# Kernel tuning notes

Measured on AMD Instinct MI355X. Metric: run time of the kernel, lower is better.

## Reference

```python
import jax, jax.numpy as jnp
import numpy as np

B = 16384
D1 = 256
D2 = 256
D_FF = 1024
N_BINS = 16
TAIL = 3.0
MIN_VAL = 1e-3
MIN_TOTAL = N_BINS * MIN_VAL
TAIL_CONST = float(np.log(np.exp(1.0 - MIN_VAL) - 1.0))
D_OUT = (3 * N_BINS - 1) * D2  # 12032


def setup_inputs() -> dict:
    key = jax.random.key(0)
    ks = jax.random.split(key, 8)
    s = lambda fan: 1.0 / np.sqrt(fan)
    return {
        'x1': jax.random.normal(ks[0], (B, D1), jnp.float32),
        'x2': jax.random.normal(ks[1], (B, D2), jnp.float32),
        'W0': jax.random.normal(ks[2], (D1, D_FF), jnp.float32) * s(D1),
        'b0': jnp.zeros((D_FF,), jnp.float32),
        'W1': jax.random.normal(ks[3], (D_FF, D_FF), jnp.float32) * s(D_FF),
        'b1': jnp.zeros((D_FF,), jnp.float32),
        'W2': jax.random.normal(ks[4], (D_FF, D_OUT), jnp.float32) * s(D_FF),
        'b2': jnp.zeros((D_OUT,), jnp.float32),
    }


def _rqs_forward(x, wu, hu, du):
    # x: [B, D2]; wu, hu: [B, D2, N_BINS]; du: [B, D2, N_BINS-1]
    widths = MIN_VAL + (1.0 - MIN_TOTAL) * jax.nn.softmax(wu, axis=-1)
    heights = MIN_VAL + (1.0 - MIN_TOTAL) * jax.nn.softmax(hu, axis=-1)
    cw = jnp.cumsum(widths, axis=-1)
    cw = jnp.concatenate([jnp.zeros_like(cw[..., :1]), cw], axis=-1)
    cw = 2.0 * TAIL * cw - TAIL  # x bin edges in [-TAIL, TAIL], [B,D2,N_BINS+1]
    ch = jnp.cumsum(heights, axis=-1)
    ch = jnp.concatenate([jnp.zeros_like(ch[..., :1]), ch], axis=-1)
    ch = 2.0 * TAIL * ch - TAIL  # y bin edges
    w = cw[..., 1:] - cw[..., :-1]
    h = ch[..., 1:] - ch[..., :-1]
    # boundary derivatives padded so softplus(TAIL_CONST)+MIN_VAL == 1 (linear tails)
    pad = jnp.full_like(du[..., :1], TAIL_CONST)
    d = MIN_VAL + jax.nn.softplus(jnp.concatenate([pad, du, pad], axis=-1))  # [B,D2,N_BINS+1]
    inside = (x > -TAIL) & (x < TAIL)
    xc = jnp.clip(x, -TAIL, TAIL)
    # data-dependent bin search against interior edges
    idx = jnp.sum((xc[..., None] >= cw[..., 1:-1]).astype(jnp.int32), axis=-1)  # [B,D2]
    take = lambda a: jnp.take_along_axis(a, idx[..., None], axis=-1)[..., 0]
    xk = take(cw[..., :-1]); yk = take(ch[..., :-1])
    wk = take(w); hk = take(h)
    dk = take(d[..., :-1]); dk1 = take(d[..., 1:])
    sk = hk / wk
    theta = (xc - xk) / wk
    t1m = theta * (1.0 - theta)
    denom = sk + (dk + dk1 - 2.0 * sk) * t1m
    y = yk + hk * (sk * theta * theta + dk * t1m) / denom
    deriv = sk * sk * (dk1 * theta * theta + 2.0 * sk * t1m + dk * (1.0 - theta) ** 2) / (denom * denom)
    y = jnp.where(inside, y, x)            # identity tails
    logdet = jnp.where(inside, jnp.log(deriv), 0.0)
    return y, jnp.sum(logdet, axis=-1)     # [B,D2], [B]


def reference(x1, x2, W0, b0, W1, b1, W2, b2):
    # conditioner MLP: x1 -> spline parameters
    hdn = jax.nn.relu(x1 @ W0 + b0)
    hdn = jax.nn.relu(hdn @ W1 + b1)
    p = (hdn @ W2 + b2).reshape(-1, D2, 3 * N_BINS - 1)
    wu = p[..., :N_BINS]
    hu = p[..., N_BINS:2 * N_BINS]
    du = p[..., 2 * N_BINS:]
    y2, logdet = _rqs_forward(x2, wu, hu, du)
    return y2, logdet
```

## Files before the change

kernel.cpp:

```cpp
#include <hip/hip_runtime.h>
#include <math.h>

using u16 = unsigned short;
using bf16x8 = __attribute__((ext_vector_type(8))) short;
using f32x4  = __attribute__((ext_vector_type(4))) float;

#define DEV static __device__ __forceinline__

DEV u16 f2bf(float f) {
  union { float f; unsigned u; } v; v.f = f;
  unsigned u = v.u + 0x7fffu + ((v.u >> 16) & 1u);
  return (u16)(u >> 16);
}

DEV void gload16(const void* g, void* l) {
  __builtin_amdgcn_global_load_lds(
      (const __attribute__((address_space(1))) void*)g,
      (__attribute__((address_space(3))) void*)l, 16, 0, 0);
}

__global__ void k_conv_bf16(const float* __restrict__ in, u16* __restrict__ out, int n) {
  int i = blockIdx.x * 256 + threadIdx.x;
  if (i < n) out[i] = f2bf(in[i]);
}

__global__ void k_transconv(const float* __restrict__ in, u16* __restrict__ out,
                            int K, int Nin, int Nout, int pack) {
  __shared__ float t[32][33];
  int kb = blockIdx.x * 32, nb = blockIdx.y * 32;
  int tx = threadIdx.x & 31, ty = threadIdx.x >> 5;
  #pragma unroll
  for (int i = 0; i < 4; ++i) {
    int k = kb + ty + i * 8;
    int no = nb + tx;
    float v = 0.f;
    if (k < K && no < Nout) {
      if (pack) {
        int r = no % 48;
        if (r < 47) v = in[(size_t)k * Nin + (no / 48) * 47 + r];
      } else {
        v = in[(size_t)k * Nin + no];
      }
    }
    t[ty + i * 8][tx] = v;
  }
  __syncthreads();
  #pragma unroll
  for (int i = 0; i < 4; ++i) {
    int no = nb + ty + i * 8;
    int k = kb + tx;
    if (no < Nout && k < K) out[(size_t)no * K + k] = f2bf(t[tx][ty + i * 8]);
  }
}

__global__ __launch_bounds__(256)
void k_gemm_relu(const u16* __restrict__ A, const u16* __restrict__ Bt,
                 const float* __restrict__ bias, u16* __restrict__ C,
                 int N, int K) {
  constexpr int BM = 128, BN = 128, BK = 32;
  __shared__ __align__(16) u16 lds[(BM + BN) * BK];
  int tid = threadIdx.x, w = tid >> 6, lane = tid & 63;
  int bn = blockIdx.x, bm = blockIdx.y;
  int brow = bm * BM, bcol = bn * BN;
  int wm = w >> 1, wn = w & 1;
  int fr = lane & 15, fg = lane >> 4;
  f32x4 acc[4][4];
  #pragma unroll
  for (int i = 0; i < 4; ++i)
    #pragma unroll
    for (int j = 0; j < 4; ++j) acc[i][j] = (f32x4){0.f, 0.f, 0.f, 0.f};

  constexpr int ACH = BM * BK / 8;
  constexpr int CALLS = (BM + BN) * BK / 8 / 64;

  for (int kt = 0; kt < K; kt += BK) {
    for (int j = 0; j * 4 + w < CALLS; ++j) {
      int cb = (j * 4 + w) * 64;
      int c = cb + lane;
      const u16* g;
      if (c < ACH) {
        int row = c >> 2, c8 = c & 3;
        g = A + (size_t)(brow + row) * K + kt + c8 * 8;
      } else {
        int b = c - ACH;
        int nn = b >> 2, c8 = b & 3;
        g = Bt + (size_t)(bcol + nn) * K + kt + c8 * 8;
      }
      gload16(g, &lds[cb * 8]);
    }
    asm volatile("s_waitcnt vmcnt(0)" ::: "memory");
    __syncthreads();

    const u16* Al = lds;
    const u16* Bl = lds + BM * BK;
    bf16x8 af[4], bfr[4];
    #pragma unroll
    for (int mi = 0; mi < 4; ++mi)
      af[mi] = *(const bf16x8*)&Al[(wm * 64 + mi * 16 + fr) * BK + fg * 8];
    #pragma unroll
    for (int ni = 0; ni < 4; ++ni)
      bfr[ni] = *(const bf16x8*)&Bl[(wn * 64 + ni * 16 + fr) * BK + fg * 8];
    #pragma unroll
    for (int mi = 0; mi < 4; ++mi)
      #pragma unroll
      for (int ni = 0; ni < 4; ++ni)
        acc[mi][ni] = __builtin_amdgcn_mfma_f32_16x16x32_bf16(af[mi], bfr[ni], acc[mi][ni], 0, 0, 0);
    __syncthreads();
  }

  #pragma unroll
  for (int ni = 0; ni < 4; ++ni) {
    int col = bcol + wn * 64 + ni * 16 + fr;
    float bb = bias[col];
    #pragma unroll
    for (int mi = 0; mi < 4; ++mi) {
      #pragma unroll
      for (int q = 0; q < 4; ++q) {
        int row = brow + wm * 64 + mi * 16 + fg * 4 + q;
        float vv = acc[mi][ni][q] + bb;
        C[(size_t)row * N + col] = f2bf(vv > 0.f ? vv : 0.f);
      }
    }
  }
}

__global__ __launch_bounds__(512, 4)
void k_gemm3_fused(const u16* __restrict__ A, const u16* __restrict__ Bt,
                   const float* __restrict__ b2, const float* __restrict__ x2,
                   float* __restrict__ y2, float* __restrict__ ldpart) {
  extern __shared__ char smem[];
  const int tid = threadIdx.x, w = tid >> 6, lane = tid & 63;
  const int wm = w >> 2, wn = w & 3;
  const int fr = lane & 15, fg = lane >> 4;

  const int bid = blockIdx.x;
  const int bm = bid >> 6;
  const int bn = ((bid & 7) << 3) | ((bid >> 3) & 7);
  const int brow = bm * 256;

  const int csrc = (tid & 3) ^ ((tid >> 2) & 3);
  const u16* gA0 = A + (size_t)(brow + (tid >> 2)) * 1024 + csrc * 8;
  const u16* gB0 = Bt + (size_t)(bn * 192 + (tid >> 2)) * 1024 + csrc * 8;

#define ISSUE_ALL(t1) {                                              \
    const size_t ko_ = (size_t)(t1) * 32;                            \
    char* pa_ = smem + ((t1) & 1) * 16384;                           \
    char* pb_ = smem + 32768 + ((t1) & 1) * 12288;                   \
    gload16(gA0 + ko_, pa_ + tid * 16);                              \
    gload16(gA0 + 131072 + ko_, pa_ + tid * 16 + 8192);              \
    if (w < 6) {                                                     \
      gload16(gB0 + ko_, pb_ + tid * 16);                            \
      gload16(gB0 + 98304 + ko_, pb_ + tid * 16 + 6144);             \
    } }

  const int sc = ((fg ^ (fr & 3)) << 4);

  f32x4 acc[8][3];
  #pragma unroll
  for (int m = 0; m < 8; ++m)
    #pragma unroll
    for (int n = 0; n < 3; ++n) acc[m][n] = (f32x4){0.f, 0.f, 0.f, 0.f};

  ISSUE_ALL(0);
  asm volatile("s_waitcnt vmcnt(0)" ::: "memory");
  __syncthreads();

  for (int t = 0; t < 32; ++t) {
    if (t < 31) ISSUE_ALL(t + 1);
    const char* Ab = smem + (t & 1) * 16384;
    const char* Bb = smem + 32768 + (t & 1) * 12288;
    bf16x8 b[3];
    #pragma unroll
    for (int n = 0; n < 3; ++n)
      b[n] = *(const bf16x8*)(Bb + (wn * 48 + n * 16 + fr) * 64 + sc);
    __builtin_amdgcn_s_setprio(1);
    #pragma unroll
    for (int m = 0; m < 8; ++m) {
      bf16x8 a = *(const bf16x8*)(Ab + (wm * 128 + m * 16 + fr) * 64 + sc);
      #pragma unroll
      for (int n = 0; n < 3; ++n)
        acc[m][n] = __builtin_amdgcn_mfma_f32_16x16x32_bf16(a, b[n], acc[m][n], 0, 0, 0);
    }
    __builtin_amdgcn_s_setprio(0);
    asm volatile("s_waitcnt vmcnt(0)" ::: "memory");
    __syncthreads();
  }

  float* ldacc = (float*)(smem + 50176);
  #pragma unroll
  for (int round = 0; round < 4; ++round) {
    const int W = round >> 1, rh = round & 1;
    if (wm == W) {
      float* slot = (float*)(smem + wn * 12544);
      #pragma unroll
      for (int mm = 0; mm < 4; ++mm)
        #pragma unroll
        for (int n = 0; n < 3; ++n)
          #pragma unroll
          for (int q = 0; q < 4; ++q)
            slot[(mm * 16 + fg * 4 + q) * 49 + n * 16 + fr] = acc[rh * 4 + mm][n][q];
    }
    __syncthreads();
    if (tid < 256) {
      const int grp = tid >> 6, r = tid & 63;
      const float* pr = (const float*)(smem + grp * 12544) + r * 49;
      const int grow = brow + W * 128 + rh * 64 + r;
      const int d2 = bn * 4 + grp;
      const float* bb = b2 + (size_t)d2 * 47;

      float wv[16], hv[16];
      #pragma unroll
      for (int j = 0; j < 16; ++j) wv[j] = pr[j] + bb[j];
      #pragma unroll
      for (int j = 0; j < 16; ++j) hv[j] = pr[16 + j] + bb[16 + j];

      float x = x2[(size_t)grow * 256 + d2];
      float xc = fminf(fmaxf(x, -3.f), 3.f);

      float mw = wv[0];
      #pragma unroll
      for (int j = 1; j < 16; ++j) mw = fmaxf(mw, wv[j]);
      float sw = 0.f;
      #pragma unroll
      for (int j = 0; j < 16; ++j) { wv[j] = __expf(wv[j] - mw); sw += wv[j]; }
      float scw = 0.984f / sw;

      float mh = hv[0];
      #pragma unroll
      for (int j = 1; j < 16; ++j) mh = fmaxf(mh, hv[j]);
      float sh = 0.f;
      #pragma unroll
      for (int j = 0; j < 16; ++j) { hv[j] = __expf(hv[j] - mh); sh += hv[j]; }
      float sch = 0.984f / sh;

      int idx = 0;
      float xk = -3.f, cum = 0.f;
      #pragma unroll
      for (int i = 1; i <= 15; ++i) {
        cum += 0.001f + wv[i - 1] * scw;
        float cwi = 6.f * cum - 3.f;
        if (xc >= cwi) { idx = i; xk = cwi; }
      }
      float yk = -3.f, cumh = 0.f;
      #pragma unroll
      for (int i = 1; i <= 15; ++i) {
        cumh += 0.001f + hv[i - 1] * sch;
        float chi = 6.f * cumh - 3.f;
        if (i == idx) yk = chi;
      }
      float wk = 1.f, hk = 1.f;
      #pragma unroll
      for (int i = 0; i < 16; ++i) {
        if (i == idx) {
          wk = 6.f * (0.001f + wv[i] * scw);
          hk = 6.f * (0.001f + hv[i] * sch);
        }
      }
      float dk = 1.f, dk1 = 1.f;
      #pragma unroll
      for (int i = 1; i <= 15; ++i) {
        float u = pr[32 + i - 1] + bb[32 + i - 1];
        float e = __expf(u);
        float dd = 0.001f + (u > 15.f ? u : log1pf(e));
        if (i == idx) dk = dd;
        if (i == idx + 1) dk1 = dd;
      }

      float sk = hk / wk;
      float th = (xc - xk) / wk;
      float om = 1.f - th;
      float t1m = th * om;
      float den = sk + (dk + dk1 - 2.f * sk) * t1m;
      float y = yk + hk * (sk * th * th + dk * t1m) / den;
      float deriv = sk * sk * (dk1 * th * th + 2.f * sk * t1m + dk * om * om) / (den * den);
      bool inside = (x > -3.f) && (x < 3.f);
      float yout = inside ? y : x;
      float ld = inside ? __logf(deriv) : 0.f;

      y2[(size_t)grow * 256 + d2] = yout;
      ldacc[(W * 128 + rh * 64 + r) * 4 + grp] = ld;
    }
    __syncthreads();
  }

  if (tid < 256) {
    float s = ldacc[tid * 4] + ldacc[tid * 4 + 1] + ldacc[tid * 4 + 2] + ldacc[tid * 4 + 3];
    ldpart[(size_t)bn * 16384 + brow + tid] = s;
  }
}

__global__ void k_reduce_ld(const float* __restrict__ part, float* __restrict__ out) {
  int r = blockIdx.x * 256 + threadIdx.x;
  float s = 0.f;
  for (int j = 0; j < 64; ++j) s += part[(size_t)j * 16384 + r];
  out[r] = s;
}

extern "C" void kernel_launch(void* const* d_in, const int* in_sizes, int n_in,
                              void* d_out, int out_size, void* d_ws, size_t ws_size,
                              hipStream_t stream) {
  const float* x1 = (const float*)d_in[0];
  const float* x2 = (const float*)d_in[1];
  const float* W0 = (const float*)d_in[2];
  const float* b0 = (const float*)d_in[3];
  const float* W1 = (const float*)d_in[4];
  const float* b1 = (const float*)d_in[5];
  const float* W2 = (const float*)d_in[6];
  const float* b2 = (const float*)d_in[7];
  float* y2 = (float*)d_out;
  float* logdet = y2 + (size_t)16384 * 256;

  char* ws = (char*)d_ws;
  u16* W2t = (u16*)ws;
  u16* W0t = (u16*)(ws + 25165824);
  u16* W1t = (u16*)(ws + 25165824 + 524288);
  u16* x1b = (u16*)(ws + 27787264);
  float* ldp = (float*)(ws + 27787264);
  u16* h1  = (u16*)(ws + 36175872);
  u16* h2  = (u16*)(ws + 69730304);

  hipFuncSetAttribute((const void*)k_gemm3_fused,
                      hipFuncAttributeMaxDynamicSharedMemorySize, 57344);

  k_conv_bf16<<<16384, 256, 0, stream>>>(x1, x1b, 16384 * 256);
  k_transconv<<<dim3(8, 32), 256, 0, stream>>>(W0, W0t, 256, 1024, 1024, 0);
  k_transconv<<<dim3(32, 32), 256, 0, stream>>>(W1, W1t, 1024, 1024, 1024, 0);
  k_transconv<<<dim3(32, 384), 256, 0, stream>>>(W2, W2t, 1024, 12032, 12288, 1);

  k_gemm_relu<<<dim3(8, 128), 256, 0, stream>>>(x1b, W0t, b0, h1, 1024, 256);
  k_gemm_relu<<<dim3(8, 128), 256, 0, stream>>>(h1, W1t, b1, h2, 1024, 1024);
  k_gemm3_fused<<<4096, 512, 57344, stream>>>(h2, W2t, b2, x2, y2, ldp);
  k_reduce_ld<<<64, 256, 0, stream>>>(ldp, logdet);
}
```

Before: 866.4 us.

## Retile final fused GEMM to 128x192 blocks with 256 threads and BK=64

The last GEMM with the fused spline epilogue now uses 128-row by 192-column tiles with 4 waves instead of 256x192 with 8 waves. The K step doubles to 64, with an 8-way XOR swizzle, which halves the loop iterations and barriers. Each wave now computes a 64x96 sub-tile, raising MFMA work per LDS read, and all 256 threads take part in the spline epilogue. In exchange, LDS per block grows to 80KB, which limits occupancy, and each B tile is read from global memory twice as often.

```diff
diff --git a/kernel.cpp b/kernel.cpp
--- a/kernel.cpp
+++ b/kernel.cpp
@@ -124,62 +124,79 @@
   }
 }
 
-__global__ __launch_bounds__(512, 4)
+__global__ __launch_bounds__(256, 2)
 void k_gemm3_fused(const u16* __restrict__ A, const u16* __restrict__ Bt,
                    const float* __restrict__ b2, const float* __restrict__ x2,
                    float* __restrict__ y2, float* __restrict__ ldpart) {
   extern __shared__ char smem[];
   const int tid = threadIdx.x, w = tid >> 6, lane = tid & 63;
-  const int wm = w >> 2, wn = w & 3;
+  const int wm = w >> 1, wn = w & 1;
   const int fr = lane & 15, fg = lane >> 4;
 
   const int bid = blockIdx.x;
   const int bm = bid >> 6;
   const int bn = ((bid & 7) << 3) | ((bid >> 3) & 7);
-  const int brow = bm * 256;
-
-  const int csrc = (tid & 3) ^ ((tid >> 2) & 3);
-  const u16* gA0 = A + (size_t)(brow + (tid >> 2)) * 1024 + csrc * 8;
-  const u16* gB0 = Bt + (size_t)(bn * 192 + (tid >> 2)) * 1024 + csrc * 8;
-
-#define ISSUE_ALL(t1) {                                              \
-    const size_t ko_ = (size_t)(t1) * 32;                            \
-    char* pa_ = smem + ((t1) & 1) * 16384;                           \
-    char* pb_ = smem + 32768 + ((t1) & 1) * 12288;                   \
-    gload16(gA0 + ko_, pa_ + tid * 16);                              \
-    gload16(gA0 + 131072 + ko_, pa_ + tid * 16 + 8192);              \
-    if (w < 6) {                                                     \
-      gload16(gB0 + ko_, pb_ + tid * 16);                            \
-      gload16(gB0 + 98304 + ko_, pb_ + tid * 16 + 6144);             \
-    } }
-
-  const int sc = ((fg ^ (fr & 3)) << 4);
-
-  f32x4 acc[8][3];
-  #pragma unroll
-  for (int m = 0; m < 8; ++m)
-    #pragma unroll
-    for (int n = 0; n < 3; ++n) acc[m][n] = (f32x4){0.f, 0.f, 0.f, 0.f};
+  const int brow = bm * 128;
+
+  const int csrc = (tid & 7) ^ ((tid >> 3) & 7);
+  const u16* gA[4]; const u16* gB[6];
+  #pragma unroll
+  for (int k = 0; k < 4; ++k)
+    gA[k] = A + (size_t)(brow + (tid >> 3) + 32 * k) * 1024 + csrc * 8;
+  #pragma unroll
+  for (int k = 0; k < 6; ++k)
+    gB[k] = Bt + (size_t)(bn * 192 + (tid >> 3) + 32 * k) * 1024 + csrc * 8;
+
+#define ISSUE_ALL(t1) {                                               \
+    const size_t ko_ = (size_t)(t1) * 64;                             \
+    char* pa_ = smem + ((t1) & 1) * 16384;                            \
+    char* pb_ = smem + 32768 + ((t1) & 1) * 24576;                    \
+    gload16(gA[0] + ko_, pa_ + tid * 16);                             \
+    gload16(gA[1] + ko_, pa_ + tid * 16 + 4096);                      \
+    gload16(gA[2] + ko_, pa_ + tid * 16 + 8192);                      \
+    gload16(gA[3] + ko_, pa_ + tid * 16 + 12288);                     \
+    gload16(gB[0] + ko_, pb_ + tid * 16);                             \
+    gload16(gB[1] + ko_, pb_ + tid * 16 + 4096);                      \
+    gload16(gB[2] + ko_, pb_ + tid * 16 + 8192);                      \
+    gload16(gB[3] + ko_, pb_ + tid * 16 + 12288);                     \
+    gload16(gB[4] + ko_, pb_ + tid * 16 + 16384);                     \
+    gload16(gB[5] + ko_, pb_ + tid * 16 + 20480); }
+
+  const int sc0 = ((fg ^ (fr & 7)) << 4);
+  const int sc1 = (((4 + fg) ^ (fr & 7)) << 4);
+
+  f32x4 acc[4][6];
+  #pragma unroll
+  for (int m = 0; m < 4; ++m)
+    #pragma unroll
+    for (int n = 0; n < 6; ++n) acc[m][n] = (f32x4){0.f, 0.f, 0.f, 0.f};
 
   ISSUE_ALL(0);
   asm volatile("s_waitcnt vmcnt(0)" ::: "memory");
   __syncthreads();
 
-  for (int t = 0; t < 32; ++t) {
-    if (t < 31) ISSUE_ALL(t + 1);
+  for (int t = 0; t < 16; ++t) {
+    if (t < 15) ISSUE_ALL(t + 1);
     const char* Ab = smem + (t & 1) * 16384;
-    const char* Bb = smem + 32768 + (t & 1) * 12288;
-    bf16x8 b[3];
-    #pragma unroll
-    for (int n = 0; n < 3; ++n)
-      b[n] = *(const bf16x8*)(Bb + (wn * 48 + n * 16 + fr) * 64 + sc);
+    const char* Bb = smem + 32768 + (t & 1) * 24576;
+    bf16x8 b0[6], b1[6];
+    #pragma unroll
+    for (int n = 0; n < 6; ++n) {
+      const char* bp = Bb + (wn * 96 + n * 16 + fr) * 128;
+      b0[n] = *(const bf16x8*)(bp + sc0);
+      b1[n] = *(const bf16x8*)(bp + sc1);
+    }
     __builtin_amdgcn_s_setprio(1);
     #pragma unroll
-    for (int m = 0; m < 8; ++m) {
-      bf16x8 a = *(const bf16x8*)(Ab + (wm * 128 + m * 16 + fr) * 64 + sc);
-      #pragma unroll
-      for (int n = 0; n < 3; ++n)
-        acc[m][n] = __builtin_amdgcn_mfma_f32_16x16x32_bf16(a, b[n], acc[m][n], 0, 0, 0);
+    for (int m = 0; m < 4; ++m) {
+      const char* ap = Ab + (wm * 64 + m * 16 + fr) * 128;
+      bf16x8 a0 = *(const bf16x8*)(ap + sc0);
+      bf16x8 a1 = *(const bf16x8*)(ap + sc1);
+      #pragma unroll
+      for (int n = 0; n < 6; ++n) {
+        acc[m][n] = __builtin_amdgcn_mfma_f32_16x16x32_bf16(a0, b0[n], acc[m][n], 0, 0, 0);
+        acc[m][n] = __builtin_amdgcn_mfma_f32_16x16x32_bf16(a1, b1[n], acc[m][n], 0, 0, 0);
+      }
     }
     __builtin_amdgcn_s_setprio(0);
     asm volatile("s_waitcnt vmcnt(0)" ::: "memory");
@@ -187,25 +204,27 @@
   }
 
   float* ldacc = (float*)(smem + 50176);
-  #pragma unroll
-  for (int round = 0; round < 4; ++round) {
-    const int W = round >> 1, rh = round & 1;
-    if (wm == W) {
-      float* slot = (float*)(smem + wn * 12544);
-      #pragma unroll
-      for (int mm = 0; mm < 4; ++mm)
+  float* fl = (float*)smem;
+  #pragma unroll
+  for (int rh = 0; rh < 2; ++rh) {
+    if (wm == rh) {
+      #pragma unroll
+      for (int m = 0; m < 4; ++m)
         #pragma unroll
-        for (int n = 0; n < 3; ++n)
+        for (int n = 0; n < 6; ++n) {
+          const int g = wn * 2 + (n >= 3 ? 1 : 0);
+          const int ci = (n % 3) * 16 + fr;
           #pragma unroll
           for (int q = 0; q < 4; ++q)
-            slot[(mm * 16 + fg * 4 + q) * 49 + n * 16 + fr] = acc[rh * 4 + mm][n][q];
-    }
-    __syncthreads();
-    if (tid < 256) {
-      const int grp = tid >> 6, r = tid & 63;
-      const float* pr = (const float*)(smem + grp * 12544) + r * 49;
-      const int grow = brow + W * 128 + rh * 64 + r;
-      const int d2 = bn * 4 + grp;
+            fl[g * 3136 + (m * 16 + fg * 4 + q) * 49 + ci] = acc[m][n][q];
+        }
+    }
+    __syncthreads();
+    {
+      const int g = tid >> 6, r = tid & 63;
+      const float* pr = fl + g * 3136 + r * 49;
+      const int grow = brow + rh * 64 + r;
+      const int d2 = bn * 4 + g;
       const float* bb = b2 + (size_t)d2 * 47;
 
       float wv[16], hv[16];
@@ -278,12 +297,12 @@
       float ld = inside ? __logf(deriv) : 0.f;
 
       y2[(size_t)grow * 256 + d2] = yout;
-      ldacc[(W * 128 + rh * 64 + r) * 4 + grp] = ld;
-    }
-    __syncthreads();
-  }
-
-  if (tid < 256) {
+      ldacc[(rh * 64 + r) * 4 + g] = ld;
+    }
+    __syncthreads();
+  }
+
+  if (tid < 128) {
     float s = ldacc[tid * 4] + ldacc[tid * 4 + 1] + ldacc[tid * 4 + 2] + ldacc[tid * 4 + 3];
     ldpart[(size_t)bn * 16384 + brow + tid] = s;
   }
@@ -320,7 +339,7 @@
   u16* h2  = (u16*)(ws + 69730304);
 
   hipFuncSetAttribute((const void*)k_gemm3_fused,
-                      hipFuncAttributeMaxDynamicSharedMemorySize, 57344);
+                      hipFuncAttributeMaxDynamicSharedMemorySize, 81920);
 
   k_conv_bf16<<<16384, 256, 0, stream>>>(x1, x1b, 16384 * 256);
   k_transconv<<<dim3(8, 32), 256, 0, stream>>>(W0, W0t, 256, 1024, 1024, 0);
@@ -329,6 +348,6 @@
 
   k_gemm_relu<<<dim3(8, 128), 256, 0, stream>>>(x1b, W0t, b0, h1, 1024, 256);
   k_gemm_relu<<<dim3(8, 128), 256, 0, stream>>>(h1, W1t, b1, h2, 1024, 1024);
-  k_gemm3_fused<<<4096, 512, 57344, stream>>>(h2, W2t, b2, x2, y2, ldp);
+  k_gemm3_fused<<<8192, 256, 81920, stream>>>(h2, W2t, b2, x2, y2, ldp);
   k_reduce_ld<<<64, 256, 0, stream>>>(ldp, logdet);
 }
```

New measurement: 736.4 us. 1.18x faster.

## Restructure final GEMM into a 192x192 tile with a three-stage 64-wide K pipeline

Applied to the files above, without the earlier changes.

Changes the fused third GEMM from 256x192 tiles with a double-buffered 32-wide K loop to 192x192 tiles with a triple-buffered 64-wide K pipeline. The wait before each barrier now only drains to vmcnt(6), so one stage's loads stay in flight during the next compute. The tile is square, the grid grows to 5504 blocks with clamping and guards on the ragged last row block, and the epilogue now handles 384 rows per round in two rounds. The kernel needs 144KB of LDS, which allows only one block per CU, so it gives up occupancy in exchange for deeper prefetch and fewer barriers.

```diff
diff --git a/kernel.cpp b/kernel.cpp
--- a/kernel.cpp
+++ b/kernel.cpp
@@ -124,7 +124,7 @@
   }
 }
 
-__global__ __launch_bounds__(512, 4)
+__global__ __launch_bounds__(512, 1)
 void k_gemm3_fused(const u16* __restrict__ A, const u16* __restrict__ Bt,
                    const float* __restrict__ b2, const float* __restrict__ x2,
                    float* __restrict__ y2, float* __restrict__ ldpart) {
@@ -136,76 +136,101 @@
   const int bid = blockIdx.x;
   const int bm = bid >> 6;
   const int bn = ((bid & 7) << 3) | ((bid >> 3) & 7);
-  const int brow = bm * 256;
-
-  const int csrc = (tid & 3) ^ ((tid >> 2) & 3);
-  const u16* gA0 = A + (size_t)(brow + (tid >> 2)) * 1024 + csrc * 8;
-  const u16* gB0 = Bt + (size_t)(bn * 192 + (tid >> 2)) * 1024 + csrc * 8;
-
-#define ISSUE_ALL(t1) {                                              \
-    const size_t ko_ = (size_t)(t1) * 32;                            \
-    char* pa_ = smem + ((t1) & 1) * 16384;                           \
-    char* pb_ = smem + 32768 + ((t1) & 1) * 12288;                   \
-    gload16(gA0 + ko_, pa_ + tid * 16);                              \
-    gload16(gA0 + 131072 + ko_, pa_ + tid * 16 + 8192);              \
-    if (w < 6) {                                                     \
-      gload16(gB0 + ko_, pb_ + tid * 16);                            \
-      gload16(gB0 + 98304 + ko_, pb_ + tid * 16 + 6144);             \
-    } }
-
-  const int sc = ((fg ^ (fr & 3)) << 4);
-
-  f32x4 acc[8][3];
-  #pragma unroll
-  for (int m = 0; m < 8; ++m)
+  const int brow = bm * 192;
+
+  const int csrc = (tid & 7) ^ ((tid >> 3) & 7);
+  const u16* gA[3]; const u16* gB[3];
+  #pragma unroll
+  for (int u = 0; u < 3; ++u) {
+    int rowA = brow + (tid >> 3) + 64 * u;
+    rowA = rowA < 16383 ? rowA : 16383;
+    gA[u] = A + (size_t)rowA * 1024 + csrc * 8;
+    gB[u] = Bt + (size_t)(bn * 192 + (tid >> 3) + 64 * u) * 1024 + csrc * 8;
+  }
+  const int ldst = tid * 16;
+
+#define STAGE(t1, sbase) {                                           \
+    const size_t ko_ = (size_t)(t1) * 64;                            \
+    char* p_ = smem + (sbase);                                       \
+    gload16(gA[0] + ko_, p_ + ldst);                                 \
+    gload16(gA[1] + ko_, p_ + 8192 + ldst);                          \
+    gload16(gA[2] + ko_, p_ + 16384 + ldst);                         \
+    gload16(gB[0] + ko_, p_ + 24576 + ldst);                         \
+    gload16(gB[1] + ko_, p_ + 32768 + ldst);                         \
+    gload16(gB[2] + ko_, p_ + 40960 + ldst); }
+
+  const int sc0 = ((fg ^ (fr & 7)) << 4);
+  const int sc1 = (((4 + fg) ^ (fr & 7)) << 4);
+
+  f32x4 acc[6][3];
+  #pragma unroll
+  for (int m = 0; m < 6; ++m)
     #pragma unroll
     for (int n = 0; n < 3; ++n) acc[m][n] = (f32x4){0.f, 0.f, 0.f, 0.f};
 
-  ISSUE_ALL(0);
-  asm volatile("s_waitcnt vmcnt(0)" ::: "memory");
+#define COMPUTE(sbase) {                                             \
+    const char* Ab_ = smem + (sbase);                                \
+    const char* Bb_ = smem + (sbase) + 24576;                        \
+    bf16x8 b0[3], b1[3];                                             \
+    _Pragma("unroll")                                                \
+    for (int n_ = 0; n_ < 3; ++n_) {                                 \
+      const char* bp_ = Bb_ + (wn * 48 + n_ * 16 + fr) * 128;        \
+      b0[n_] = *(const bf16x8*)(bp_ + sc0);                          \
+      b1[n_] = *(const bf16x8*)(bp_ + sc1);                          \
+    }                                                                \
+    __builtin_amdgcn_s_setprio(1);                                   \
+    _Pragma("unroll")                                                \
+    for (int m_ = 0; m_ < 6; ++m_) {                                 \
+      const char* ap_ = Ab_ + (wm * 96 + m_ * 16 + fr) * 128;        \
+      bf16x8 a0_ = *(const bf16x8*)(ap_ + sc0);                      \
+      bf16x8 a1_ = *(const bf16x8*)(ap_ + sc1);                      \
+      _Pragma("unroll")                                              \
+      for (int n_ = 0; n_ < 3; ++n_) {                               \
+        acc[m_][n_] = __builtin_amdgcn_mfma_f32_16x16x32_bf16(a0_, b0[n_], acc[m_][n_], 0, 0, 0); \
+        acc[m_][n_] = __builtin_amdgcn_mfma_f32_16x16x32_bf16(a1_, b1[n_], acc[m_][n_], 0, 0, 0); \
+      }                                                              \
+    }                                                                \
+    __builtin_amdgcn_s_setprio(0); }
+
+#define VMW(n) asm volatile("s_waitcnt vmcnt(" #n ")" ::: "memory")
+
+  STAGE(0, 0); STAGE(1, 49152);
+  VMW(6);
+  __builtin_amdgcn_s_barrier();
+
+  for (int j = 0; j < 4; ++j) {
+    const int t = j * 3;
+    STAGE(t + 2, 98304); COMPUTE(0);     VMW(6); __builtin_amdgcn_s_barrier();
+    STAGE(t + 3, 0);     COMPUTE(49152); VMW(6); __builtin_amdgcn_s_barrier();
+    STAGE(t + 4, 49152); COMPUTE(98304); VMW(6); __builtin_amdgcn_s_barrier();
+  }
+  STAGE(14, 98304); COMPUTE(0); VMW(6); __builtin_amdgcn_s_barrier();
+  STAGE(15, 0);     COMPUTE(49152); VMW(6); __builtin_amdgcn_s_barrier();
+  COMPUTE(98304); VMW(0); __builtin_amdgcn_s_barrier();
+  COMPUTE(0);
   __syncthreads();
 
-  for (int t = 0; t < 32; ++t) {
-    if (t < 31) ISSUE_ALL(t + 1);
-    const char* Ab = smem + (t & 1) * 16384;
-    const char* Bb = smem + 32768 + (t & 1) * 12288;
-    bf16x8 b[3];
-    #pragma unroll
-    for (int n = 0; n < 3; ++n)
-      b[n] = *(const bf16x8*)(Bb + (wn * 48 + n * 16 + fr) * 64 + sc);
-    __builtin_amdgcn_s_setprio(1);
-    #pragma unroll
-    for (int m = 0; m < 8; ++m) {
-      bf16x8 a = *(const bf16x8*)(Ab + (wm * 128 + m * 16 + fr) * 64 + sc);
-      #pragma unroll
-      for (int n = 0; n < 3; ++n)
-        acc[m][n] = __builtin_amdgcn_mfma_f32_16x16x32_bf16(a, b[n], acc[m][n], 0, 0, 0);
-    }
-    __builtin_amdgcn_s_setprio(0);
-    asm volatile("s_waitcnt vmcnt(0)" ::: "memory");
-    __syncthreads();
-  }
-
-  float* ldacc = (float*)(smem + 50176);
-  #pragma unroll
-  for (int round = 0; round < 4; ++round) {
-    const int W = round >> 1, rh = round & 1;
-    if (wm == W) {
-      float* slot = (float*)(smem + wn * 12544);
-      #pragma unroll
-      for (int mm = 0; mm < 4; ++mm)
+  float* fl = (float*)smem;
+  float* ldacc = (float*)(smem + 75264);
+  #pragma unroll
+  for (int r = 0; r < 2; ++r) {
+    if ((wn >> 1) == r) {
+      float* slot = fl + (wn & 1) * 9408;
+      #pragma unroll
+      for (int m = 0; m < 6; ++m)
         #pragma unroll
         for (int n = 0; n < 3; ++n)
           #pragma unroll
           for (int q = 0; q < 4; ++q)
-            slot[(mm * 16 + fg * 4 + q) * 49 + n * 16 + fr] = acc[rh * 4 + mm][n][q];
+            slot[(wm * 96 + m * 16 + fg * 4 + q) * 49 + n * 16 + fr] = acc[m][n][q];
     }
     __syncthreads();
-    if (tid < 256) {
-      const int grp = tid >> 6, r = tid & 63;
-      const float* pr = (const float*)(smem + grp * 12544) + r * 49;
-      const int grow = brow + W * 128 + rh * 64 + r;
-      const int d2 = bn * 4 + grp;
+    if (tid < 384) {
+      const int g01 = (tid >= 192) ? 1 : 0;
+      const int rr = tid - g01 * 192;
+      const int grow = brow + rr;
+      const int d2 = bn * 4 + r * 2 + g01;
+      const float* pr = fl + g01 * 9408 + rr * 49;
       const float* bb = b2 + (size_t)d2 * 47;
 
       float wv[16], hv[16];
@@ -214,7 +239,7 @@
       #pragma unroll
       for (int j = 0; j < 16; ++j) hv[j] = pr[16 + j] + bb[16 + j];
 
-      float x = x2[(size_t)grow * 256 + d2];
+      float x = (grow < 16384) ? x2[(size_t)grow * 256 + d2] : 0.f;
       float xc = fminf(fmaxf(x, -3.f), 3.f);
 
       float mw = wv[0];
@@ -277,15 +302,20 @@
       float yout = inside ? y : x;
       float ld = inside ? __logf(deriv) : 0.f;
 
-      y2[(size_t)grow * 256 + d2] = yout;
-      ldacc[(W * 128 + rh * 64 + r) * 4 + grp] = ld;
+      if (grow < 16384) {
+        y2[(size_t)grow * 256 + d2] = yout;
+        ldacc[rr * 4 + r * 2 + g01] = ld;
+      }
     }
     __syncthreads();
   }
 
-  if (tid < 256) {
-    float s = ldacc[tid * 4] + ldacc[tid * 4 + 1] + ldacc[tid * 4 + 2] + ldacc[tid * 4 + 3];
-    ldpart[(size_t)bn * 16384 + brow + tid] = s;
+  if (tid < 192) {
+    int grow = brow + tid;
+    if (grow < 16384) {
+      float s = ldacc[tid * 4] + ldacc[tid * 4 + 1] + ldacc[tid * 4 + 2] + ldacc[tid * 4 + 3];
+      ldpart[(size_t)bn * 16384 + grow] = s;
+    }
   }
 }
 
@@ -320,7 +350,7 @@
   u16* h2  = (u16*)(ws + 69730304);
 
   hipFuncSetAttribute((const void*)k_gemm3_fused,
-                      hipFuncAttributeMaxDynamicSharedMemorySize, 57344);
+                      hipFuncAttributeMaxDynamicSharedMemorySize, 147456);
 
   k_conv_bf16<<<16384, 256, 0, stream>>>(x1, x1b, 16384 * 256);
   k_transconv<<<dim3(8, 32), 256, 0, stream>>>(W0, W0t, 256, 1024, 1024, 0);
@@ -329,6 +359,6 @@
 
   k_gemm_relu<<<dim3(8, 128), 256, 0, stream>>>(x1b, W0t, b0, h1, 1024, 256);
   k_gemm_relu<<<dim3(8, 128), 256, 0, stream>>>(h1, W1t, b1, h2, 1024, 1024);
-  k_gemm3_fused<<<4096, 512, 57344, stream>>>(h2, W2t, b2, x2, y2, ldp);
+  k_gemm3_fused<<<5504, 512, 147456, stream>>>(h2, W2t, b2, x2, y2, ldp);
   k_reduce_ld<<<64, 256, 0, stream>>>(ldp, logdet);
 }
```

After: 889.3 us. 2.6% more time.

## Enlarge fused GEMM3 tile to 256x384 with 1024 threads and triple-buffered LDS

Applied to the files above, without the earlier changes.

The fused output GEMM now uses 1024-thread blocks computing 256x384 tiles (eight spline dims per block instead of four), halving the number of blocks and the partial log-det columns. Global-to-LDS loads move from double to triple buffering with partial vmcnt waits, so the next two stages stay in flight during compute, and the LDS swizzle changes to suit the new layout. The spline epilogue is split across 512 threads in four rounds. This raises arithmetic intensity and load/compute overlap, at the cost of 120KB LDS per block, which leaves one block per CU and fewer blocks overall.

```diff
diff --git a/kernel.cpp b/kernel.cpp
--- a/kernel.cpp
+++ b/kernel.cpp
@@ -124,7 +124,7 @@
   }
 }
 
-__global__ __launch_bounds__(512, 4)
+__global__ __launch_bounds__(1024, 4)
 void k_gemm3_fused(const u16* __restrict__ A, const u16* __restrict__ Bt,
                    const float* __restrict__ b2, const float* __restrict__ x2,
                    float* __restrict__ y2, float* __restrict__ ldpart) {
@@ -134,78 +134,90 @@
   const int fr = lane & 15, fg = lane >> 4;
 
   const int bid = blockIdx.x;
-  const int bm = bid >> 6;
-  const int bn = ((bid & 7) << 3) | ((bid >> 3) & 7);
+  const int bm = bid >> 5;
+  const int bn = ((bid & 7) << 2) | ((bid >> 3) & 3);
   const int brow = bm * 256;
 
-  const int csrc = (tid & 3) ^ ((tid >> 2) & 3);
-  const u16* gA0 = A + (size_t)(brow + (tid >> 2)) * 1024 + csrc * 8;
-  const u16* gB0 = Bt + (size_t)(bn * 192 + (tid >> 2)) * 1024 + csrc * 8;
-
-#define ISSUE_ALL(t1) {                                              \
-    const size_t ko_ = (size_t)(t1) * 32;                            \
-    char* pa_ = smem + ((t1) & 1) * 16384;                           \
-    char* pb_ = smem + 32768 + ((t1) & 1) * 12288;                   \
-    gload16(gA0 + ko_, pa_ + tid * 16);                              \
-    gload16(gA0 + 131072 + ko_, pa_ + tid * 16 + 8192);              \
-    if (w < 6) {                                                     \
-      gload16(gB0 + ko_, pb_ + tid * 16);                            \
-      gload16(gB0 + 98304 + ko_, pb_ + tid * 16 + 6144);             \
-    } }
-
-  const int sc = ((fg ^ (fr & 3)) << 4);
-
-  f32x4 acc[8][3];
-  #pragma unroll
-  for (int m = 0; m < 8; ++m)
-    #pragma unroll
-    for (int n = 0; n < 3; ++n) acc[m][n] = (f32x4){0.f, 0.f, 0.f, 0.f};
-
-  ISSUE_ALL(0);
+  const int csrc = (tid & 3) ^ ((tid >> 3) & 3);
+  const u16* gA  = A  + (size_t)(brow + (tid >> 2)) * 1024 + csrc * 8;
+  const u16* gB1 = Bt + (size_t)(bn * 384 + (tid >> 2)) * 1024 + csrc * 8;
+  const u16* gB2 = Bt + (size_t)(bn * 384 + 256 + (tid >> 2)) * 1024 + csrc * 8;
+
+#define STAGE(t1, sb) {                                               \
+    const size_t ko_ = (size_t)(t1) * 32;                             \
+    char* p_ = smem + (sb);                                           \
+    gload16(gA + ko_, p_ + tid * 16);                                 \
+    gload16(gB1 + ko_, p_ + 16384 + tid * 16);                        \
+    if (tid < 512) gload16(gB2 + ko_, p_ + 32768 + tid * 16); }
+
+#define VMW_T() { if (w < 8) asm volatile("s_waitcnt vmcnt(3)" ::: "memory"); \
+                  else       asm volatile("s_waitcnt vmcnt(2)" ::: "memory"); }
+#define BARRIER() { __builtin_amdgcn_sched_barrier(0); __builtin_amdgcn_s_barrier(); \
+                    __builtin_amdgcn_sched_barrier(0); }
+
+  const int sc = ((fg ^ ((fr >> 1) & 3)) << 4);
+  const int abase = (wm * 64 + fr) * 64 + sc;
+  const int bbase = (wn * 96 + fr) * 64 + sc;
+
+  f32x4 acc[4][6];
+  #pragma unroll
+  for (int m = 0; m < 4; ++m)
+    #pragma unroll
+    for (int n = 0; n < 6; ++n) acc[m][n] = (f32x4){0.f, 0.f, 0.f, 0.f};
+
+#define COMPUTE(sb) {                                                 \
+    const char* Ab_ = smem + (sb);                                    \
+    const char* Bb_ = smem + (sb) + 16384;                            \
+    bf16x8 a_[4];                                                     \
+    _Pragma("unroll")                                                 \
+    for (int m_ = 0; m_ < 4; ++m_)                                    \
+      a_[m_] = *(const bf16x8*)(Ab_ + abase + m_ * 1024);             \
+    __builtin_amdgcn_s_setprio(1);                                    \
+    _Pragma("unroll")                                                 \
+    for (int n_ = 0; n_ < 6; ++n_) {                                  \
+      bf16x8 b_ = *(const bf16x8*)(Bb_ + bbase + n_ * 1024);          \
+      _Pragma("unroll")                                               \
+      for (int m_ = 0; m_ < 4; ++m_)                                  \
+        acc[m_][n_] = __builtin_amdgcn_mfma_f32_16x16x32_bf16(a_[m_], b_, acc[m_][n_], 0, 0, 0); \
+    }                                                                 \
+    __builtin_amdgcn_s_setprio(0); }
+
+  STAGE(0, 0); STAGE(1, 40960);
+  VMW_T();
+  BARRIER();
+
+  for (int j = 0; j < 10; ++j) {
+    STAGE(3 * j + 2, 81920); COMPUTE(0);     VMW_T(); BARRIER();
+    STAGE(3 * j + 3, 0);     COMPUTE(40960); VMW_T(); BARRIER();
+    STAGE(3 * j + 4, 40960); COMPUTE(81920); VMW_T(); BARRIER();
+  }
+  COMPUTE(0);
   asm volatile("s_waitcnt vmcnt(0)" ::: "memory");
+  BARRIER();
+  COMPUTE(40960);
   __syncthreads();
 
-  for (int t = 0; t < 32; ++t) {
-    if (t < 31) ISSUE_ALL(t + 1);
-    const char* Ab = smem + (t & 1) * 16384;
-    const char* Bb = smem + 32768 + (t & 1) * 12288;
-    bf16x8 b[3];
-    #pragma unroll
-    for (int n = 0; n < 3; ++n)
-      b[n] = *(const bf16x8*)(Bb + (wn * 48 + n * 16 + fr) * 64 + sc);
-    __builtin_amdgcn_s_setprio(1);
-    #pragma unroll
-    for (int m = 0; m < 8; ++m) {
-      bf16x8 a = *(const bf16x8*)(Ab + (wm * 128 + m * 16 + fr) * 64 + sc);
-      #pragma unroll
-      for (int n = 0; n < 3; ++n)
-        acc[m][n] = __builtin_amdgcn_mfma_f32_16x16x32_bf16(a, b[n], acc[m][n], 0, 0, 0);
-    }
-    __builtin_amdgcn_s_setprio(0);
-    asm volatile("s_waitcnt vmcnt(0)" ::: "memory");
-    __syncthreads();
-  }
-
-  float* ldacc = (float*)(smem + 50176);
-  #pragma unroll
-  for (int round = 0; round < 4; ++round) {
-    const int W = round >> 1, rh = round & 1;
-    if (wm == W) {
-      float* slot = (float*)(smem + wn * 12544);
-      #pragma unroll
-      for (int mm = 0; mm < 4; ++mm)
+  float* fl = (float*)smem;
+  float* ldacc = (float*)(smem + 100352);
+  #pragma unroll
+  for (int r = 0; r < 4; ++r) {
+    const int rh2 = r >> 1, pp = r & 1;
+    if ((wm >> 1) == rh2) {
+      float* slot = fl + wn * (128 * 49);
+      #pragma unroll
+      for (int m = 0; m < 4; ++m)
         #pragma unroll
-        for (int n = 0; n < 3; ++n)
+        for (int j = 0; j < 3; ++j)
           #pragma unroll
           for (int q = 0; q < 4; ++q)
-            slot[(mm * 16 + fg * 4 + q) * 49 + n * 16 + fr] = acc[rh * 4 + mm][n][q];
+            slot[((wm & 1) * 64 + m * 16 + fg * 4 + q) * 49 + j * 16 + fr] = acc[m][pp * 3 + j][q];
     }
     __syncthreads();
-    if (tid < 256) {
-      const int grp = tid >> 6, r = tid & 63;
-      const float* pr = (const float*)(smem + grp * 12544) + r * 49;
-      const int grow = brow + W * 128 + rh * 64 + r;
-      const int d2 = bn * 4 + grp;
+    if (tid < 512) {
+      const int g = tid >> 7, rr = tid & 127;
+      const float* pr = fl + g * (128 * 49) + rr * 49;
+      const int grow = brow + rh2 * 128 + rr;
+      const int d2 = bn * 8 + g * 2 + pp;
       const float* bb = b2 + (size_t)d2 * 47;
 
       float wv[16], hv[16];
@@ -278,13 +290,15 @@
       float ld = inside ? __logf(deriv) : 0.f;
 
       y2[(size_t)grow * 256 + d2] = yout;
-      ldacc[(W * 128 + rh * 64 + r) * 4 + grp] = ld;
+      ldacc[(rh2 * 128 + rr) * 8 + g * 2 + pp] = ld;
     }
     __syncthreads();
   }
 
   if (tid < 256) {
-    float s = ldacc[tid * 4] + ldacc[tid * 4 + 1] + ldacc[tid * 4 + 2] + ldacc[tid * 4 + 3];
+    float s = 0.f;
+    #pragma unroll
+    for (int g = 0; g < 8; ++g) s += ldacc[tid * 8 + g];
     ldpart[(size_t)bn * 16384 + brow + tid] = s;
   }
 }
@@ -292,7 +306,7 @@
 __global__ void k_reduce_ld(const float* __restrict__ part, float* __restrict__ out) {
   int r = blockIdx.x * 256 + threadIdx.x;
   float s = 0.f;
-  for (int j = 0; j < 64; ++j) s += part[(size_t)j * 16384 + r];
+  for (int j = 0; j < 32; ++j) s += part[(size_t)j * 16384 + r];
   out[r] = s;
 }
 
@@ -320,7 +334,7 @@
   u16* h2  = (u16*)(ws + 69730304);
 
   hipFuncSetAttribute((const void*)k_gemm3_fused,
-                      hipFuncAttributeMaxDynamicSharedMemorySize, 57344);
+                      hipFuncAttributeMaxDynamicSharedMemorySize, 122880);
 
   k_conv_bf16<<<16384, 256, 0, stream>>>(x1, x1b, 16384 * 256);
   k_transconv<<<dim3(8, 32), 256, 0, stream>>>(W0, W0t, 256, 1024, 1024, 0);
@@ -329,6 +343,6 @@
 
   k_gemm_relu<<<dim3(8, 128), 256, 0, stream>>>(x1b, W0t, b0, h1, 1024, 256);
   k_gemm_relu<<<dim3(8, 128), 256, 0, stream>>>(h1, W1t, b1, h2, 1024, 1024);
-  k_gemm3_fused<<<4096, 512, 57344, stream>>>(h2, W2t, b2, x2, y2, ldp);
+  k_gemm3_fused<<<2048, 1024, 122880, stream>>>(h2, W2t, b2, x2, y2, ldp);
   k_reduce_ld<<<64, 256, 0, stream>>>(ldp, logdet);
 }
```

After: 2.221 ms. 156% more time.
